# Performance work log

Hardware: AMD Instinct MI355X
Metric: run time of the kernel (lower is better)

## Reference

```python
import jax, jax.numpy as jnp
import numpy as np

B, I, O, C, U = 32, 2048, 32, 16, 32  # batch, in_channels(caps), out_capsules, in_capsules(dim), unit_size
NUM_ITERS = 3


def setup_inputs() -> dict:
    key = jax.random.key(0)
    k1, k2 = jax.random.split(key)
    x = jax.random.normal(k1, (B, I, C), dtype=jnp.float32)
    w = jax.random.normal(k2, (I, O, C, U), dtype=jnp.float32)
    return {"x": x, "w": w}


def _squash(v):
    # faithful to original: vec * |vec| / (1 + |vec|^2), norm over last (unit) dim
    n = jnp.linalg.norm(v, axis=-1, keepdims=True)
    return v * n / (1.0 + n * n)


def reference(x, w):
    # u_hat[b,i,o,u] = sum_c x[b,i,c] * w[i,o,c,u]   (the original's x @ w with singleton dims dropped)
    u_hat = jnp.einsum('bic,iocu->biou', x, w)  # [B,I,O,U]
    b_log = jnp.zeros((I, O, 1), dtype=x.dtype)
    v = None
    for _ in range(NUM_ITERS):
        # original computes softmax over dim=2 of [I,O,1] (a singleton dim) -> all ones; kept faithful
        c = jax.nn.softmax(b_log, axis=2)[..., 0]  # [I,O]
        s = jnp.einsum('io,biou->bou', c, u_hat)   # sum over input capsules
        v = _squash(s)                              # [B,O,U]
        # agreement: per-(b,i,o) dot(u_hat, v), then mean over batch (original's update.mean(dim=0))
        agree = jnp.einsum('biou,bou->io', u_hat, v) / B
        b_log = b_log + agree[..., None]
    return v[:, :, None, :]  # matches original v.squeeze(1) -> [B, O, 1, U]
```

## Files before the change

kernel.cpp:

```cpp
#include <hip/hip_runtime.h>
#include <math.h>

#define B_   32
#define I_   2048
#define O_   32
#define C_   16
#define U_   32
#define NCOL (O_ * U_)
#define TI   4
#define NBLK (I_ / TI)
#define SLICE (B_ * NCOL)
#define BH   16
#define XS   36


__global__ __launch_bounds__(512, 4) void caps_partial(const float* __restrict__ x,
                                                       const float* __restrict__ w,
                                                       float* __restrict__ ws) {
    __shared__ float xs[TI * C_ * XS];
    const int tid = threadIdx.x;
    const int i0 = blockIdx.x * TI;

    for (int k = tid; k < B_ * TI * C_; k += 512) {
        int b   = k >> 6;
        int rem = k & 63;
        xs[rem * XS + b] = x[(size_t)b * (I_ * C_) + (size_t)i0 * C_ + rem];
    }
    __syncthreads();

    const int bh = tid >> 8;
    const int ct = tid & 255;
    const int o  = ct >> 3;
    const int u4 = (ct & 7) << 2;
    const float* wp = w + (size_t)i0 * (O_ * C_ * U_) + o * (C_ * U_) + u4;

    float4 acc[BH];
#pragma unroll
    for (int b = 0; b < BH; ++b) acc[b] = make_float4(0.f, 0.f, 0.f, 0.f);

    for (int il = 0; il < TI; ++il) {
        const float* wpi = wp + (size_t)il * (O_ * C_ * U_);
        const float* xr  = &xs[il * C_ * XS + bh * BH];
#pragma unroll
        for (int cc = 0; cc < C_; cc += 4) {
            float4 wv[4];
#pragma unroll
            for (int j = 0; j < 4; ++j)
                wv[j] = *(const float4*)(wpi + (cc + j) * U_);
#pragma unroll
            for (int j = 0; j < 4; ++j) {
                const float4* xv = (const float4*)(xr + (cc + j) * XS);
#pragma unroll
                for (int q = 0; q < 4; ++q) {
                    float4 xq = xv[q];
                    float4* a = &acc[q * 4];
                    a[0].x = fmaf(xq.x, wv[j].x, a[0].x);
                    a[0].y = fmaf(xq.x, wv[j].y, a[0].y);
                    a[0].z = fmaf(xq.x, wv[j].z, a[0].z);
                    a[0].w = fmaf(xq.x, wv[j].w, a[0].w);
                    a[1].x = fmaf(xq.y, wv[j].x, a[1].x);
                    a[1].y = fmaf(xq.y, wv[j].y, a[1].y);
                    a[1].z = fmaf(xq.y, wv[j].z, a[1].z);
                    a[1].w = fmaf(xq.y, wv[j].w, a[1].w);
                    a[2].x = fmaf(xq.z, wv[j].x, a[2].x);
                    a[2].y = fmaf(xq.z, wv[j].y, a[2].y);
                    a[2].z = fmaf(xq.z, wv[j].z, a[2].z);
                    a[2].w = fmaf(xq.z, wv[j].w, a[2].w);
                    a[3].x = fmaf(xq.w, wv[j].x, a[3].x);
                    a[3].y = fmaf(xq.w, wv[j].y, a[3].y);
                    a[3].z = fmaf(xq.w, wv[j].z, a[3].z);
                    a[3].w = fmaf(xq.w, wv[j].w, a[3].w);
                }
            }
        }
    }

    float* op = ws + (size_t)blockIdx.x * SLICE + (size_t)(bh * BH) * NCOL + o * U_ + u4;
#pragma unroll
    for (int b = 0; b < BH; ++b)
        *(float4*)(op + (size_t)b * NCOL) = acc[b];
}

__global__ __launch_bounds__(256) void caps_reduce_squash(const float* __restrict__ ws,
                                                          float* __restrict__ out) {
    __shared__ float sh[128];
    const int tl = threadIdx.x & 127;
    const int ph = threadIdx.x >> 7;
    const int t  = blockIdx.x * 128 + tl;
    const float* p = ws + (size_t)ph * (NBLK / 2) * SLICE + t;
    float s = 0.f;
#pragma unroll 16
    for (int i = 0; i < NBLK / 2; ++i)
        s += p[(size_t)i * SLICE];
    if (ph) sh[tl] = s;
    __syncthreads();
    if (ph == 0) {
        s += sh[tl];
        float ss = s * s;
        ss += __shfl_xor(ss, 1);
        ss += __shfl_xor(ss, 2);
        ss += __shfl_xor(ss, 4);
        ss += __shfl_xor(ss, 8);
        ss += __shfl_xor(ss, 16);
        float n = sqrtf(ss);
        out[t] = s * n / (1.0f + ss);
    }
}

__global__ __launch_bounds__(256, 2) void caps_main_atomic(const float* __restrict__ x,
                                                           const float* __restrict__ w,
                                                           float* __restrict__ out) {
    __shared__ float xs[TI * C_ * 33];
    const int tid = threadIdx.x;
    const int i0 = blockIdx.x * TI;
    for (int k = tid; k < B_ * TI * C_; k += 256) {
        int b = k >> 6, rem = k & 63;
        xs[rem * 33 + b] = x[(size_t)b * (I_ * C_) + (size_t)i0 * C_ + rem];
    }
    __syncthreads();
    const int o = tid >> 3, u4 = (tid & 7) << 2;
    const float* wp = w + (size_t)i0 * (O_ * C_ * U_) + o * (C_ * U_) + u4;
    float4 acc[B_];
#pragma unroll
    for (int b = 0; b < B_; ++b) acc[b] = make_float4(0.f, 0.f, 0.f, 0.f);
    for (int il = 0; il < TI; ++il) {
        const float* wpi = wp + (size_t)il * (O_ * C_ * U_);
        const float* xr = &xs[il * C_ * 33];
#pragma unroll
        for (int c = 0; c < C_; ++c) {
            float4 wv = *(const float4*)(wpi + c * U_);
            const float* xc = xr + c * 33;
#pragma unroll
            for (int b = 0; b < B_; ++b) {
                float xb = xc[b];
                acc[b].x = fmaf(xb, wv.x, acc[b].x);
                acc[b].y = fmaf(xb, wv.y, acc[b].y);
                acc[b].z = fmaf(xb, wv.z, acc[b].z);
                acc[b].w = fmaf(xb, wv.w, acc[b].w);
            }
        }
    }
    float* op = out + o * U_ + u4;
#pragma unroll
    for (int b = 0; b < B_; ++b) {
        float* p = op + (size_t)b * NCOL;
        atomicAdd(p + 0, acc[b].x);
        atomicAdd(p + 1, acc[b].y);
        atomicAdd(p + 2, acc[b].z);
        atomicAdd(p + 3, acc[b].w);
    }
}

__global__ void caps_squash_inplace(float* __restrict__ out) {
    int t = blockIdx.x * 256 + threadIdx.x;
    float s = out[t];
    float ss = s * s;
    ss += __shfl_xor(ss, 1);
    ss += __shfl_xor(ss, 2);
    ss += __shfl_xor(ss, 4);
    ss += __shfl_xor(ss, 8);
    ss += __shfl_xor(ss, 16);
    float n = sqrtf(ss);
    out[t] = s * n / (1.0f + ss);
}

extern "C" void kernel_launch(void* const* d_in, const int* in_sizes, int n_in,
                              void* d_out, int out_size, void* d_ws, size_t ws_size,
                              hipStream_t stream) {
    const float* x = (const float*)d_in[0];
    const float* w = (const float*)d_in[1];
    float* out = (float*)d_out;

    const size_t need = (size_t)NBLK * SLICE * sizeof(float);
    if (ws_size >= need) {
        float* ws = (float*)d_ws;
        caps_partial<<<NBLK, 512, 0, stream>>>(x, w, ws);
        caps_reduce_squash<<<SLICE / 128, 256, 0, stream>>>(ws, out);
    } else {
        hipMemsetAsync(out, 0, (size_t)SLICE * sizeof(float), stream);
        caps_main_atomic<<<I_ / TI, 256, 0, stream>>>(x, w, out);
        caps_squash_inplace<<<SLICE / 256, 256, 0, stream>>>(out);
    }
}
```

Before: 211.8 us.

## Double input-capsule tile and split columns across blocks to shrink partial workspace

Each block now covers 8 input capsules but only a quarter of the output columns, with each thread holding 4 batch rows instead of 16. This halves the number of partial-sum slices written to the workspace and later read by the reduce kernel, cutting memory traffic. It also raises occupancy through smaller per-thread accumulators. The cost is lower register-level reuse per shared-memory x load and a larger x staging tile per block.

```diff
diff --git a/kernel.cpp b/kernel.cpp
--- a/kernel.cpp
+++ b/kernel.cpp
@@ -6,41 +6,43 @@
 #define O_   32
 #define C_   16
 #define U_   32
-#define NCOL (O_ * U_)
-#define TI   4
-#define NBLK (I_ / TI)
+#define NCOL  (O_ * U_)
+#define TI    8
+#define NIG   (I_ / TI)
+#define CQ    4
 #define SLICE (B_ * NCOL)
-#define BH   16
-#define XS   36
+#define XS    36
 
 
-__global__ __launch_bounds__(512, 4) void caps_partial(const float* __restrict__ x,
+__global__ __launch_bounds__(512, 8) void caps_partial(const float* __restrict__ x,
                                                        const float* __restrict__ w,
                                                        float* __restrict__ ws) {
     __shared__ float xs[TI * C_ * XS];
     const int tid = threadIdx.x;
-    const int i0 = blockIdx.x * TI;
+    const int ig  = blockIdx.x >> 2;
+    const int cq  = blockIdx.x & 3;
+    const int i0  = ig * TI;
 
     for (int k = tid; k < B_ * TI * C_; k += 512) {
-        int b   = k >> 6;
-        int rem = k & 63;
+        int b   = k >> 7;
+        int rem = k & 127;
         xs[rem * XS + b] = x[(size_t)b * (I_ * C_) + (size_t)i0 * C_ + rem];
     }
     __syncthreads();
 
-    const int bh = tid >> 8;
-    const int ct = tid & 255;
-    const int o  = ct >> 3;
-    const int u4 = (ct & 7) << 2;
-    const float* wp = w + (size_t)i0 * (O_ * C_ * U_) + o * (C_ * U_) + u4;
+    const int colf4 = tid & 63;
+    const int bg    = tid >> 6;
+    const int o     = cq * 8 + (colf4 >> 3);
+    const int u4    = (colf4 & 7) << 2;
+    const float* wp = w + o * (C_ * U_) + u4;
 
-    float4 acc[BH];
+    float4 acc[4];
 #pragma unroll
-    for (int b = 0; b < BH; ++b) acc[b] = make_float4(0.f, 0.f, 0.f, 0.f);
+    for (int b = 0; b < 4; ++b) acc[b] = make_float4(0.f, 0.f, 0.f, 0.f);
 
     for (int il = 0; il < TI; ++il) {
-        const float* wpi = wp + (size_t)il * (O_ * C_ * U_);
-        const float* xr  = &xs[il * C_ * XS + bh * BH];
+        const float* wpi = wp + (size_t)(i0 + il) * (O_ * C_ * U_);
+        const float* xr  = &xs[il * C_ * XS + bg * 4];
 #pragma unroll
         for (int cc = 0; cc < C_; cc += 4) {
             float4 wv[4];
@@ -49,35 +51,30 @@
                 wv[j] = *(const float4*)(wpi + (cc + j) * U_);
 #pragma unroll
             for (int j = 0; j < 4; ++j) {
-                const float4* xv = (const float4*)(xr + (cc + j) * XS);
-#pragma unroll
-                for (int q = 0; q < 4; ++q) {
-                    float4 xq = xv[q];
-                    float4* a = &acc[q * 4];
-                    a[0].x = fmaf(xq.x, wv[j].x, a[0].x);
-                    a[0].y = fmaf(xq.x, wv[j].y, a[0].y);
-                    a[0].z = fmaf(xq.x, wv[j].z, a[0].z);
-                    a[0].w = fmaf(xq.x, wv[j].w, a[0].w);
-                    a[1].x = fmaf(xq.y, wv[j].x, a[1].x);
-                    a[1].y = fmaf(xq.y, wv[j].y, a[1].y);
-                    a[1].z = fmaf(xq.y, wv[j].z, a[1].z);
-                    a[1].w = fmaf(xq.y, wv[j].w, a[1].w);
-                    a[2].x = fmaf(xq.z, wv[j].x, a[2].x);
-                    a[2].y = fmaf(xq.z, wv[j].y, a[2].y);
-                    a[2].z = fmaf(xq.z, wv[j].z, a[2].z);
-                    a[2].w = fmaf(xq.z, wv[j].w, a[2].w);
-                    a[3].x = fmaf(xq.w, wv[j].x, a[3].x);
-                    a[3].y = fmaf(xq.w, wv[j].y, a[3].y);
-                    a[3].z = fmaf(xq.w, wv[j].z, a[3].z);
-                    a[3].w = fmaf(xq.w, wv[j].w, a[3].w);
-                }
+                float4 xq = *(const float4*)(xr + (cc + j) * XS);
+                acc[0].x = fmaf(xq.x, wv[j].x, acc[0].x);
+                acc[0].y = fmaf(xq.x, wv[j].y, acc[0].y);
+                acc[0].z = fmaf(xq.x, wv[j].z, acc[0].z);
+                acc[0].w = fmaf(xq.x, wv[j].w, acc[0].w);
+                acc[1].x = fmaf(xq.y, wv[j].x, acc[1].x);
+                acc[1].y = fmaf(xq.y, wv[j].y, acc[1].y);
+                acc[1].z = fmaf(xq.y, wv[j].z, acc[1].z);
+                acc[1].w = fmaf(xq.y, wv[j].w, acc[1].w);
+                acc[2].x = fmaf(xq.z, wv[j].x, acc[2].x);
+                acc[2].y = fmaf(xq.z, wv[j].y, acc[2].y);
+                acc[2].z = fmaf(xq.z, wv[j].z, acc[2].z);
+                acc[2].w = fmaf(xq.z, wv[j].w, acc[2].w);
+                acc[3].x = fmaf(xq.w, wv[j].x, acc[3].x);
+                acc[3].y = fmaf(xq.w, wv[j].y, acc[3].y);
+                acc[3].z = fmaf(xq.w, wv[j].z, acc[3].z);
+                acc[3].w = fmaf(xq.w, wv[j].w, acc[3].w);
             }
         }
     }
 
-    float* op = ws + (size_t)blockIdx.x * SLICE + (size_t)(bh * BH) * NCOL + o * U_ + u4;
+    float* op = ws + (size_t)ig * SLICE + (size_t)(bg * 4) * NCOL + cq * 256 + colf4 * 4;
 #pragma unroll
-    for (int b = 0; b < BH; ++b)
+    for (int b = 0; b < 4; ++b)
         *(float4*)(op + (size_t)b * NCOL) = acc[b];
 }
 
@@ -87,10 +84,10 @@
     const int tl = threadIdx.x & 127;
     const int ph = threadIdx.x >> 7;
     const int t  = blockIdx.x * 128 + tl;
-    const float* p = ws + (size_t)ph * (NBLK / 2) * SLICE + t;
+    const float* p = ws + (size_t)ph * (NIG / 2) * SLICE + t;
     float s = 0.f;
 #pragma unroll 16
-    for (int i = 0; i < NBLK / 2; ++i)
+    for (int i = 0; i < NIG / 2; ++i)
         s += p[(size_t)i * SLICE];
     if (ph) sh[tl] = s;
     __syncthreads();
@@ -110,12 +107,12 @@
 __global__ __launch_bounds__(256, 2) void caps_main_atomic(const float* __restrict__ x,
                                                            const float* __restrict__ w,
                                                            float* __restrict__ out) {
-    __shared__ float xs[TI * C_ * 33];
+    __shared__ float xsf[4 * C_ * 33];
     const int tid = threadIdx.x;
-    const int i0 = blockIdx.x * TI;
-    for (int k = tid; k < B_ * TI * C_; k += 256) {
+    const int i0 = blockIdx.x * 4;
+    for (int k = tid; k < B_ * 4 * C_; k += 256) {
         int b = k >> 6, rem = k & 63;
-        xs[rem * 33 + b] = x[(size_t)b * (I_ * C_) + (size_t)i0 * C_ + rem];
+        xsf[rem * 33 + b] = x[(size_t)b * (I_ * C_) + (size_t)i0 * C_ + rem];
     }
     __syncthreads();
     const int o = tid >> 3, u4 = (tid & 7) << 2;
@@ -123,9 +120,9 @@
     float4 acc[B_];
 #pragma unroll
     for (int b = 0; b < B_; ++b) acc[b] = make_float4(0.f, 0.f, 0.f, 0.f);
-    for (int il = 0; il < TI; ++il) {
+    for (int il = 0; il < 4; ++il) {
         const float* wpi = wp + (size_t)il * (O_ * C_ * U_);
-        const float* xr = &xs[il * C_ * 33];
+        const float* xr = &xsf[il * C_ * 33];
 #pragma unroll
         for (int c = 0; c < C_; ++c) {
             float4 wv = *(const float4*)(wpi + c * U_);
@@ -171,14 +168,14 @@
     const float* w = (const float*)d_in[1];
     float* out = (float*)d_out;
 
-    const size_t need = (size_t)NBLK * SLICE * sizeof(float);
+    const size_t need = (size_t)NIG * SLICE * sizeof(float);
     if (ws_size >= need) {
         float* ws = (float*)d_ws;
-        caps_partial<<<NBLK, 512, 0, stream>>>(x, w, ws);
+        caps_partial<<<NIG * CQ, 512, 0, stream>>>(x, w, ws);
         caps_reduce_squash<<<SLICE / 128, 256, 0, stream>>>(ws, out);
     } else {
         hipMemsetAsync(out, 0, (size_t)SLICE * sizeof(float), stream);
-        caps_main_atomic<<<I_ / TI, 256, 0, stream>>>(x, w, out);
+        caps_main_atomic<<<I_ / 4, 256, 0, stream>>>(x, w, out);
         caps_squash_inplace<<<SLICE / 256, 256, 0, stream>>>(out);
     }
 }
```

Result: slower. 275.0 us (+29.8%).
